# Performance work log

Measured on AMD Instinct MI355X. Metric: run time of the kernel, lower is better.

## Reference

```python
import jax, jax.numpy as jnp
import numpy as np

HEADS = 8
EPS = 1e-6

def _feature_map(x):
    return jax.nn.elu(x) + 1.0

def _linear_attention(q, k, v, motion_weight):
    # q,k,v: [..., N, dh]; motion_weight broadcastable to q or None
    q = _feature_map(q)
    k = _feature_map(k)
    if motion_weight is not None:
        q = q * motion_weight
    k_sum = k.sum(axis=-2, keepdims=True)                      # [...,1,dh]
    kv = jnp.einsum('...nd,...ne->...de', k, v)                # [...,dh,dh]
    out = jnp.einsum('...nd,...de->...ne', q, kv)              # [...,N,dh]
    z = 1.0 / (jnp.einsum('...nd,...md->...nm', q, k_sum) + EPS)  # [...,N,1]
    return out * z

def setup_inputs() -> dict:
    key = jax.random.key(0)
    k1, k2, k3, k4 = jax.random.split(key, 4)
    B, T, H, W, C = 2, 16, 48, 48, 512
    x = jax.random.normal(k1, (B, T, H, W, C), dtype=jnp.float32)
    motion_mag = jax.random.normal(k2, (B, T, H, W, 1), dtype=jnp.float32)
    W_qkv = jax.random.normal(k3, (C, 3 * C), dtype=jnp.float32) * 0.02
    temporal_emb = jax.random.normal(k4, (1, 1, 1, 1, C), dtype=jnp.float32)
    return {"x": x, "motion_mag": motion_mag, "W_qkv": W_qkv, "temporal_emb": temporal_emb}

def _split_heads(t, lead, n, heads, dh):
    # t: [lead, n, heads*dh] -> [lead, heads, n, dh]
    return t.reshape(lead, n, heads, dh).transpose(0, 2, 1, 3)

def reference(x, motion_mag, W_qkv, temporal_emb):
    B, T, H, W, C = x.shape
    dh = C // HEADS
    x = x + temporal_emb

    # ---- temporal linear attention over frame-averaged tokens ----
    x_time = x.reshape(B, T, H * W, C).mean(axis=2)            # [B,T,C]
    qkv = x_time @ W_qkv                                       # [B,T,3C]
    q, k, v = jnp.split(qkv, 3, axis=-1)
    q = _split_heads(q, B, T, HEADS, dh)                       # [B,h,T,dh]
    k = _split_heads(k, B, T, HEADS, dh)
    v = _split_heads(v, B, T, HEADS, dh)
    mm = motion_mag.reshape(B, T, -1).mean(axis=-1, keepdims=True)  # [B,T,1]
    mw_t = 1.0 + jnp.tanh(mm)[:, None]                         # [B,1,T,1]
    t_out = _linear_attention(q, k, v, mw_t)                   # [B,h,T,dh]
    t_out = t_out.transpose(0, 2, 1, 3).reshape(B, T, C)       # [B,T,C]

    # broadcast temporal output over spatial dims
    x_sp = x + t_out[:, :, None, None, :]                      # [B,T,H,W,C]

    # ---- global spatial linear attention per frame ----
    N = H * W
    x_flat = x_sp.reshape(B * T, N, C)
    qkv = x_flat @ W_qkv                                       # [BT,N,3C]
    q, k, v = jnp.split(qkv, 3, axis=-1)
    q = _split_heads(q, B * T, N, HEADS, dh)                   # [BT,h,N,dh]
    k = _split_heads(k, B * T, N, HEADS, dh)
    v = _split_heads(v, B * T, N, HEADS, dh)
    mm2 = motion_mag.reshape(B * T, N, 1)
    mw_s = 1.0 + jnp.tanh(mm2)[:, None]                        # [BT,1,N,1]
    s_out = _linear_attention(q, k, v, mw_s)                   # [BT,h,N,dh]
    s_out = s_out.transpose(0, 2, 1, 3).reshape(B, T, H, W, C)
    return s_out
```

## Files before the change

kernel.cpp:

```cpp
#include <hip/hip_runtime.h>
#include <cstddef>
#include <cstdint>

#define HEADS 8
#define DH 64
#define C 512
#define TC 1536
#define BT 32
#define NTOK 2304
#define TT 16
#define EPS 1e-6f

typedef __attribute__((ext_vector_type(8))) short bf16x8;
typedef __attribute__((ext_vector_type(4))) float f32x4;
typedef __attribute__((address_space(3))) void as3_void;
typedef __attribute__((address_space(1))) const void as1_cvoid;

__device__ __forceinline__ float fmap(float x) {
    return x > 0.f ? x + 1.f : __expf(x);
}
__device__ __forceinline__ unsigned short f2bf(float f) {
    unsigned int u = __float_as_uint(f);
    return (unsigned short)((u + 0x7fffu + ((u >> 16) & 1u)) >> 16);
}
__device__ __forceinline__ unsigned int pack2bf(float a, float b) {
    return (unsigned int)f2bf(a) | ((unsigned int)f2bf(b) << 16);
}
__device__ __forceinline__ float bf2f(unsigned short h) {
    return __uint_as_float(((unsigned int)h) << 16);
}
__device__ __forceinline__ void gload16(const void* g, void* l) {
    __builtin_amdgcn_global_load_lds((as1_cvoid*)(uintptr_t)g,
                                     (as3_void*)(uintptr_t)l, 16, 0, 0);
}

__global__ __launch_bounds__(256) void k_prep_w(
    const float* __restrict__ W, unsigned short* __restrict__ Wt) {
    __shared__ float tile[32][33];
    int col0 = blockIdx.x * 32, c0 = blockIdx.y * 32;
    int tx = threadIdx.x & 31, ty = threadIdx.x >> 5;
#pragma unroll
    for (int j = 0; j < 4; ++j) {
        int c = ty + j * 8;
        tile[c][tx] = W[(size_t)(c0 + c) * TC + col0 + tx];
    }
    __syncthreads();
#pragma unroll
    for (int j = 0; j < 4; ++j) {
        int col = ty + j * 8;
        Wt[(size_t)(col0 + col) * C + c0 + tx] = f2bf(tile[tx][col]);
    }
}

__global__ __launch_bounds__(256) void k_time_reduce(
    const float* __restrict__ x, const float* __restrict__ motion,
    float* __restrict__ xtraw, float* __restrict__ mmraw,
    unsigned short* __restrict__ xb) {
    int bt = blockIdx.x, sp = blockIdx.y, tid = threadIdx.x;
    int n0 = sp * 288, cid = tid * 2;
    const float* xp = x + ((size_t)(bt * NTOK + n0)) * C + cid;
    unsigned short* xbp = xb + ((size_t)(bt * NTOK + n0)) * C + cid;
    float s0 = 0.f, s1 = 0.f;
    for (int n = 0; n < 288; ++n) {
        float2 v = *(const float2*)(xp + (size_t)n * C);
        s0 += v.x;
        s1 += v.y;
        *(unsigned int*)(xbp + (size_t)n * C) = pack2bf(v.x, v.y);
    }
    atomicAdd(&xtraw[bt * C + cid], s0);
    atomicAdd(&xtraw[bt * C + cid + 1], s1);

    const float* mp = motion + (size_t)bt * NTOK + n0;
    float m = mp[tid];
    if (tid < 32) m += mp[256 + tid];
    __shared__ float red[256];
    red[tid] = m;
    __syncthreads();
    for (int s = 128; s > 0; s >>= 1) {
        if (tid < s) red[tid] += red[tid + s];
        __syncthreads();
    }
    if (tid == 0) atomicAdd(&mmraw[bt], red[0]);
}

__global__ __launch_bounds__(256) void k_time_qkv(
    const float* __restrict__ xtraw, const float* __restrict__ temb,
    const float* __restrict__ W, float* __restrict__ qkvt) {
    int bt = blockIdx.x, col = blockIdx.y * 256 + threadIdx.x, tid = threadIdx.x;
    __shared__ float xl[C];
    xl[tid]       = xtraw[bt * C + tid]       * (1.f / NTOK) + temb[tid];
    xl[tid + 256] = xtraw[bt * C + tid + 256] * (1.f / NTOK) + temb[tid + 256];
    __syncthreads();
    float a = 0.f;
#pragma unroll 8
    for (int c = 0; c < C; ++c) a += xl[c] * W[(size_t)c * TC + col];
    qkvt[(size_t)bt * TC + col] = a;
}

__global__ __launch_bounds__(256) void k_time_attn(
    const float* __restrict__ qkvt, const float* __restrict__ mmraw,
    const float* __restrict__ temb, float* __restrict__ bias) {
    int b = blockIdx.x, h = blockIdx.y, tid = threadIdx.x;
    int d = tid & 63, g = tid >> 6;
    __shared__ float qs[TT][DH], ks[TT][DH], vs[TT][DH], ksum[DH];
    __shared__ float kvl[DH][DH];
    for (int t = g; t < TT; t += 4) {
        size_t base = (size_t)(b * TT + t) * TC + h * DH + d;
        float mwt = 1.f + tanhf(mmraw[b * TT + t] * (1.f / NTOK));
        qs[t][d] = fmap(qkvt[base]) * mwt;
        ks[t][d] = fmap(qkvt[base + C]);
        vs[t][d] = qkvt[base + 2 * C];
    }
    __syncthreads();
    if (g == 0) {
        float s = 0.f;
        for (int t = 0; t < TT; ++t) s += ks[t][d];
        ksum[d] = s;
    }
    float kva[16];
#pragma unroll
    for (int i = 0; i < 16; ++i) kva[i] = 0.f;
    for (int t = 0; t < TT; ++t) {
        float kd = ks[t][d];
#pragma unroll
        for (int i = 0; i < 16; ++i) kva[i] += kd * vs[t][g * 16 + i];
    }
#pragma unroll
    for (int i = 0; i < 16; ++i) kvl[d][g * 16 + i] = kva[i];
    __syncthreads();
    for (int tt = 0; tt < 4; ++tt) {
        int t = g * 4 + tt;
        float acc = 0.f, zden = 0.f;
        for (int dd = 0; dd < DH; ++dd) {
            float qv = qs[t][dd];
            acc  += qv * kvl[dd][d];
            zden += qv * ksum[dd];
        }
        bias[(size_t)(b * TT + t) * C + h * DH + d] =
            acc / (zden + EPS) + temb[h * DH + d];
    }
}

__global__ __launch_bounds__(256) void k_bias_vec(
    const float* __restrict__ bias, const float* __restrict__ W,
    float* __restrict__ bvec) {
    int bt = blockIdx.x, col = blockIdx.y * 256 + threadIdx.x, tid = threadIdx.x;
    __shared__ float bl[C];
    bl[tid]       = bias[bt * C + tid];
    bl[tid + 256] = bias[bt * C + tid + 256];
    __syncthreads();
    float a = 0.f;
#pragma unroll 8
    for (int c = 0; c < C; ++c) a += bl[c] * W[(size_t)c * TC + col];
    bvec[(size_t)bt * TC + col] = a;
}

__global__ __launch_bounds__(512) void k_spatial_kv(
    const unsigned short* __restrict__ xb, const unsigned short* __restrict__ Wt,
    const float* __restrict__ bvec, float* __restrict__ kvw,
    float* __restrict__ ksw) {
    __shared__ __align__(16) char smem[50176];
    unsigned short* A_s = (unsigned short*)smem;
    unsigned short* B_s = (unsigned short*)(smem + 16384);
    char* kvT = smem;
    float* bvl = (float*)(smem + 49152);

    const int s = blockIdx.x, hp = blockIdx.y, bt = blockIdx.z;
    const int tid = threadIdx.x, lane = tid & 63, w = tid >> 6;
    const int lm = lane & 15, quad = lane >> 4;
    const int mr = w & 1, nc = w >> 1;
    const int li8 = lane >> 3, lp = lane & 7;

    if (tid < 256) {
        int h2 = tid >> 7, j2 = tid & 127;
        int wr = (j2 < 64) ? (C + (hp * 2 + h2) * DH + j2)
                           : (2 * C + (hp * 2 + h2) * DH + (j2 - 64));
        bvl[tid] = bvec[(size_t)bt * TC + wr];
    }
    float ksp0 = 0.f, ksp1 = 0.f;
    f32x4 kvacc[2][2];
#pragma unroll
    for (int a = 0; a < 2; ++a)
#pragma unroll
        for (int b = 0; b < 2; ++b) kvacc[a][b] = (f32x4)0.f;

    for (int t = 0; t < 3; ++t) {
        const int n0 = (s * 3 + t) * 128;
        f32x4 acc[4][4];
#pragma unroll
        for (int i = 0; i < 4; ++i)
#pragma unroll
            for (int j = 0; j < 4; ++j) acc[i][j] = (f32x4)0.f;

        for (int kc = 0; kc < 8; ++kc) {
            __syncthreads();
#pragma unroll
            for (int l = 0; l < 2; ++l) {
                int rowbase = w * 16 + l * 8;
                int row = rowbase + li8;
                int c = lp ^ (row & 7);
                gload16(xb + ((size_t)(bt * NTOK + n0 + row)) * C + kc * 64 + c * 8,
                        A_s + rowbase * 64);
            }
#pragma unroll
            for (int l = 0; l < 4; ++l) {
                int rowbase = w * 32 + l * 8;
                int r = rowbase + li8;
                int c = lp ^ (r & 7);
                int h2 = r >> 7, j2 = r & 127;
                int wr = (j2 < 64) ? (C + (hp * 2 + h2) * DH + j2)
                                   : (2 * C + (hp * 2 + h2) * DH + (j2 - 64));
                gload16(Wt + (size_t)wr * C + kc * 64 + c * 8, B_s + rowbase * 64);
            }
            __syncthreads();
#pragma unroll
            for (int ks = 0; ks < 2; ++ks) {
                bf16x8 af[4], bfr[4];
#pragma unroll
                for (int i = 0; i < 4; ++i) {
                    int row = mr * 64 + i * 16 + lm;
                    int p = (ks * 4 + quad) ^ (row & 7);
                    af[i] = *(const bf16x8*)&A_s[row * 64 + p * 8];
                }
#pragma unroll
                for (int j = 0; j < 4; ++j) {
                    int row = nc * 64 + j * 16 + lm;
                    int p = (ks * 4 + quad) ^ (row & 7);
                    bfr[j] = *(const bf16x8*)&B_s[row * 64 + p * 8];
                }
#pragma unroll
                for (int i = 0; i < 4; ++i)
#pragma unroll
                    for (int j = 0; j < 4; ++j)
                        acc[i][j] = __builtin_amdgcn_mfma_f32_16x16x32_bf16(
                            af[i], bfr[j], acc[i][j], 0, 0, 0);
            }
        }
#pragma unroll 1
        for (int ph = 0; ph < 2; ++ph) {
            __syncthreads();
            if ((nc >> 1) == ph) {
#pragma unroll
                for (int i = 0; i < 4; ++i) {
                    int tokb = mr * 64 + i * 16 + quad * 4;
                    int tc = tokb >> 3;
#pragma unroll
                    for (int j = 0; j < 4; ++j) {
                        int cg = nc * 64 + j * 16 + lm;
                        int cl = cg & 127;
                        float bv = bvl[cg];
                        f32x4 a4 = acc[i][j];
                        float v0 = a4[0] + bv, v1 = a4[1] + bv;
                        float v2 = a4[2] + bv, v3 = a4[3] + bv;
                        if (cl < 64) {
                            v0 = fmap(v0); v1 = fmap(v1);
                            v2 = fmap(v2); v3 = fmap(v3);
                        }
                        int p = (tc & 8) | ((tc & 7) ^ (cl & 7));
                        uint2 pk;
                        pk.x = pack2bf(v0, v1);
                        pk.y = pack2bf(v2, v3);
                        *(uint2*)(kvT + cl * 256 + p * 16 + (tokb & 7) * 2) = pk;
                    }
                }
            }
            __syncthreads();
            if (tid < 128) {
                int d = tid & 63, half = tid >> 6;
                float ssum = 0.f;
#pragma unroll
                for (int tc2 = 0; tc2 < 8; ++tc2) {
                    int tcc = half * 8 + tc2;
                    int p = (tcc & 8) | ((tcc & 7) ^ (d & 7));
                    bf16x8 v8 = *(const bf16x8*)(kvT + d * 256 + p * 16);
#pragma unroll
                    for (int q = 0; q < 8; ++q)
                        ssum += bf2f((unsigned short)v8[q]);
                }
                if (ph == 0) ksp0 += ssum; else ksp1 += ssum;
            }
#pragma unroll
            for (int dt2 = 0; dt2 < 2; ++dt2) {
                int drow = (mr * 2 + dt2) * 16 + lm;
                int erow = 64 + nc * 16 + lm;
#pragma unroll
                for (int ks2 = 0; ks2 < 4; ++ks2) {
                    int tcc = ks2 * 4 + quad;
                    int pA = (tcc & 8) | ((tcc & 7) ^ (drow & 7));
                    int pB = (tcc & 8) | ((tcc & 7) ^ (erow & 7));
                    bf16x8 ak = *(const bf16x8*)(kvT + drow * 256 + pA * 16);
                    bf16x8 bv8 = *(const bf16x8*)(kvT + erow * 256 + pB * 16);
                    kvacc[ph][dt2] = __builtin_amdgcn_mfma_f32_16x16x32_bf16(
                        ak, bv8, kvacc[ph][dt2], 0, 0, 0);
                }
            }
        }
    }
#pragma unroll
    for (int ph = 0; ph < 2; ++ph) {
        float* kvp = kvw + (size_t)(bt * HEADS + hp * 2 + ph) * DH * DH;
#pragma unroll
        for (int dt2 = 0; dt2 < 2; ++dt2) {
            int d0 = (mr * 2 + dt2) * 16 + quad * 4;
            int e = nc * 16 + lm;
#pragma unroll
            for (int r = 0; r < 4; ++r)
                atomicAdd(&kvp[(d0 + r) * DH + e], kvacc[ph][dt2][r]);
        }
    }
    if (tid < 128) {
        int d = tid & 63;
        atomicAdd(&ksw[(bt * HEADS + hp * 2 + 0) * DH + d], ksp0);
        atomicAdd(&ksw[(bt * HEADS + hp * 2 + 1) * DH + d], ksp1);
    }
}

__global__ __launch_bounds__(256) void k_spatial_out(
    const unsigned short* __restrict__ xb, const unsigned short* __restrict__ Wt,
    const float* __restrict__ bvec, const float* __restrict__ motion,
    const float* __restrict__ kvw, const float* __restrict__ ksw,
    float* __restrict__ out) {
    __shared__ __align__(16) char smem[51712];
    unsigned short* A_s = (unsigned short*)smem;
    unsigned short* B_s = (unsigned short*)(smem + 16384);
    char* qs  = smem;
    char* kvT = smem + 32768;
    float* bvl = (float*)(smem + 49152);
    float* mwv = (float*)(smem + 49664);
    float* ksl = (float*)(smem + 50176);
    float* zv  = (float*)(smem + 50688);

    const int tile = blockIdx.x, hp = blockIdx.y, bt = blockIdx.z;
    const int tid = threadIdx.x, lane = tid & 63, w = tid >> 6;
    const int lm = lane & 15, quad = lane >> 4;
    const int mr = w & 1, nc = w >> 1;
    const int li8 = lane >> 3, lp = lane & 7;
    const int n0 = tile * 128;

    if (tid < 128) {
        bvl[tid] = bvec[(size_t)bt * TC + hp * 128 + tid];
        mwv[tid] = 1.f + tanhf(motion[(size_t)bt * NTOK + n0 + tid]);
        ksl[tid] = ksw[(bt * HEADS + hp * 2 + (tid >> 6)) * DH + (tid & 63)];
    }
    {
        int rr = tid & 127, hh = tid >> 7;
        int head = rr >> 6, e = rr & 63;
        const float* kvp = kvw + (size_t)(bt * HEADS + hp * 2 + head) * DH * DH;
#pragma unroll 8
        for (int d = hh * 32; d < hh * 32 + 32; ++d) {
            int p = (d >> 3) ^ (rr & 7);
            ((unsigned short*)(kvT + rr * 128 + p * 16))[d & 7] = f2bf(kvp[d * DH + e]);
        }
    }
    f32x4 acc[4][4];
#pragma unroll
    for (int i = 0; i < 4; ++i)
#pragma unroll
        for (int j = 0; j < 4; ++j) acc[i][j] = (f32x4)0.f;

    for (int kc = 0; kc < 8; ++kc) {
        __syncthreads();
#pragma unroll
        for (int l = 0; l < 4; ++l) {
            int rowbase = w * 32 + l * 8;
            int row = rowbase + li8;
            int c = lp ^ (row & 7);
            gload16(xb + ((size_t)(bt * NTOK + n0 + row)) * C + kc * 64 + c * 8,
                    A_s + rowbase * 64);
        }
#pragma unroll
        for (int l = 0; l < 4; ++l) {
            int rowbase = w * 32 + l * 8;
            int r = rowbase + li8;
            int c = lp ^ (r & 7);
            gload16(Wt + (size_t)(hp * 128 + r) * C + kc * 64 + c * 8,
                    B_s + rowbase * 64);
        }
        __syncthreads();
#pragma unroll
        for (int ks = 0; ks < 2; ++ks) {
            bf16x8 af[4], bfr[4];
#pragma unroll
            for (int i = 0; i < 4; ++i) {
                int row = mr * 64 + i * 16 + lm;
                int p = (ks * 4 + quad) ^ (row & 7);
                af[i] = *(const bf16x8*)&A_s[row * 64 + p * 8];
            }
#pragma unroll
            for (int j = 0; j < 4; ++j) {
                int row = nc * 64 + j * 16 + lm;
                int p = (ks * 4 + quad) ^ (row & 7);
                bfr[j] = *(const bf16x8*)&B_s[row * 64 + p * 8];
            }
#pragma unroll
            for (int i = 0; i < 4; ++i)
#pragma unroll
                for (int j = 0; j < 4; ++j)
                    acc[i][j] = __builtin_amdgcn_mfma_f32_16x16x32_bf16(
                        af[i], bfr[j], acc[i][j], 0, 0, 0);
        }
    }
    __syncthreads();
#pragma unroll
    for (int i = 0; i < 4; ++i) {
#pragma unroll
        for (int j = 0; j < 4; ++j) {
            int cl = nc * 64 + j * 16 + lm;
            float bv = bvl[cl];
            int cch = cl >> 3;
#pragma unroll
            for (int r = 0; r < 4; ++r) {
                int tok = mr * 64 + i * 16 + quad * 4 + r;
                float qv = fmap(acc[i][j][r] + bv) * mwv[tok];
                int p = (cch & 8) | ((cch & 7) ^ (tok & 7));
                ((unsigned short*)(qs + tok * 256 + p * 16))[cl & 7] = f2bf(qv);
            }
        }
    }
    __syncthreads();
    {
        int head = tid >> 7, tok = tid & 127;
        float zd = 0.f;
#pragma unroll
        for (int tc3 = 0; tc3 < 8; ++tc3) {
            int cch = head * 8 + tc3;
            int p = (cch & 8) | ((cch & 7) ^ (tok & 7));
            bf16x8 q8 = *(const bf16x8*)(qs + tok * 256 + p * 16);
#pragma unroll
            for (int q = 0; q < 8; ++q)
                zd += bf2f((unsigned short)q8[q]) * ksl[head * 64 + tc3 * 8 + q];
        }
        zv[head * 128 + tok] = 1.f / (zd + EPS);
    }
    __syncthreads();
    f32x4 oacc[4][4];
#pragma unroll
    for (int i = 0; i < 4; ++i)
#pragma unroll
        for (int j = 0; j < 4; ++j) oacc[i][j] = (f32x4)0.f;
#pragma unroll
    for (int ks3 = 0; ks3 < 2; ++ks3) {
        bf16x8 aq[4], bk[4];
#pragma unroll
        for (int i = 0; i < 4; ++i) {
            int tok = mr * 64 + i * 16 + lm;
            int cch = nc * 8 + ks3 * 4 + quad;
            int p = (cch & 8) | ((cch & 7) ^ (tok & 7));
            aq[i] = *(const bf16x8*)(qs + tok * 256 + p * 16);
        }
#pragma unroll
        for (int j = 0; j < 4; ++j) {
            int row = nc * 64 + j * 16 + lm;
            int tcc = ks3 * 4 + quad;
            int p = tcc ^ (row & 7);
            bk[j] = *(const bf16x8*)(kvT + row * 128 + p * 16);
        }
#pragma unroll
        for (int i = 0; i < 4; ++i)
#pragma unroll
            for (int j = 0; j < 4; ++j)
                oacc[i][j] = __builtin_amdgcn_mfma_f32_16x16x32_bf16(
                    aq[i], bk[j], oacc[i][j], 0, 0, 0);
    }
    const int h = hp * 2 + nc;
#pragma unroll
    for (int i = 0; i < 4; ++i)
#pragma unroll
        for (int r = 0; r < 4; ++r) {
            int tok = mr * 64 + i * 16 + quad * 4 + r;
            float z = zv[nc * 128 + tok];
#pragma unroll
            for (int j = 0; j < 4; ++j)
                out[((size_t)(bt * NTOK + n0 + tok)) * C + h * DH + j * 16 + lm] =
                    oacc[i][j][r] * z;
        }
}

extern "C" void kernel_launch(void* const* d_in, const int* in_sizes, int n_in,
                              void* d_out, int out_size, void* d_ws, size_t ws_size,
                              hipStream_t stream) {
    (void)in_sizes; (void)n_in; (void)out_size; (void)ws_size;
    const float* x      = (const float*)d_in[0];
    const float* motion = (const float*)d_in[1];
    const float* W      = (const float*)d_in[2];
    const float* temb   = (const float*)d_in[3];
    float* out = (float*)d_out;
    float* ws  = (float*)d_ws;

    float* kvw   = ws;
    float* ksw   = kvw + 1048576;
    float* xtraw = ksw + 16384;
    float* mmraw = xtraw + 16384;
    float* qkvt  = mmraw + 32;
    float* bias  = qkvt + 49152;
    float* bvec  = bias + 16384;
    unsigned short* Wt = (unsigned short*)(bvec + 49152);
    unsigned short* xb = (unsigned short*)(Wt + (size_t)TC * C);

    hipMemsetAsync(d_ws, 0,
                   (size_t)(1048576 + 16384 + 16384 + 32) * sizeof(float), stream);
    k_prep_w<<<dim3(48, 16), 256, 0, stream>>>(W, Wt);
    k_time_reduce<<<dim3(BT, 8), 256, 0, stream>>>(x, motion, xtraw, mmraw, xb);
    k_time_qkv<<<dim3(BT, 6), 256, 0, stream>>>(xtraw, temb, W, qkvt);
    k_time_attn<<<dim3(2, HEADS), 256, 0, stream>>>(qkvt, mmraw, temb, bias);
    k_bias_vec<<<dim3(BT, 6), 256, 0, stream>>>(bias, W, bvec);
    k_spatial_kv<<<dim3(6, 4, BT), 512, 0, stream>>>(xb, Wt, bvec, kvw, ksw);
    k_spatial_out<<<dim3(18, 4, BT), 256, 0, stream>>>(xb, Wt, bvec, motion,
                                                       kvw, ksw, out);
}
```

Measured before the change: 573.3 us.

## Double-buffer LDS tiles in spatial KV GEMM to overlap loads with MFMA

Adds a second LDS buffer for the A and B tiles in k_spatial_kv so the global-to-LDS load for the next K chunk is issued before the MFMAs on the current chunk. Source pointers are precomputed once, and the kv transpose staging is moved to a different LDS offset. This aims to hide global load latency behind matrix math and removes one barrier per K step. In exchange LDS use roughly doubles to about 97KB per block, which can lower occupancy, and it adds a barrier after each tile.

```diff
diff --git a/kernel.cpp b/kernel.cpp
--- a/kernel.cpp
+++ b/kernel.cpp
@@ -159,11 +159,13 @@
     const unsigned short* __restrict__ xb, const unsigned short* __restrict__ Wt,
     const float* __restrict__ bvec, float* __restrict__ kvw,
     float* __restrict__ ksw) {
-    __shared__ __align__(16) char smem[50176];
-    unsigned short* A_s = (unsigned short*)smem;
-    unsigned short* B_s = (unsigned short*)(smem + 16384);
-    char* kvT = smem;
-    float* bvl = (float*)(smem + 49152);
+    __shared__ __align__(16) char smem[99328];
+    unsigned short* A0 = (unsigned short*)smem;
+    unsigned short* B0 = (unsigned short*)(smem + 16384);
+    unsigned short* A1 = (unsigned short*)(smem + 49152);
+    unsigned short* B1 = (unsigned short*)(smem + 65536);
+    char* kvT = smem + 16384;
+    float* bvl = (float*)(smem + 98304);
 
     const int s = blockIdx.x, hp = blockIdx.y, bt = blockIdx.z;
     const int tid = threadIdx.x, lane = tid & 63, w = tid >> 6;
@@ -177,6 +179,24 @@
                            : (2 * C + (hp * 2 + h2) * DH + (j2 - 64));
         bvl[tid] = bvec[(size_t)bt * TC + wr];
     }
+    const unsigned short* srcA[2];
+#pragma unroll
+    for (int l = 0; l < 2; ++l) {
+        int row = w * 16 + l * 8 + li8;
+        int c = lp ^ (row & 7);
+        srcA[l] = xb + ((size_t)(bt * NTOK + row)) * C + c * 8;
+    }
+    const unsigned short* srcB[4];
+#pragma unroll
+    for (int l = 0; l < 4; ++l) {
+        int r = w * 32 + l * 8 + li8;
+        int c = lp ^ (r & 7);
+        int h2 = r >> 7, j2 = r & 127;
+        int wr = (j2 < 64) ? (C + (hp * 2 + h2) * DH + j2)
+                           : (2 * C + (hp * 2 + h2) * DH + (j2 - 64));
+        srcB[l] = Wt + (size_t)wr * C + c * 8;
+    }
+
     float ksp0 = 0.f, ksp1 = 0.f;
     f32x4 kvacc[2][2];
 #pragma unroll
@@ -184,6 +204,16 @@
 #pragma unroll
         for (int b = 0; b < 2; ++b) kvacc[a][b] = (f32x4)0.f;
 
+    auto STAGE = [&](unsigned short* As, unsigned short* Bs, int n0, int kc) {
+#pragma unroll
+        for (int l = 0; l < 2; ++l)
+            gload16(srcA[l] + (size_t)n0 * C + kc * 64, As + (w * 16 + l * 8) * 64);
+#pragma unroll
+        for (int l = 0; l < 4; ++l)
+            gload16(srcB[l] + kc * 64, Bs + (w * 32 + l * 8) * 64);
+    };
+
+#pragma unroll 1
     for (int t = 0; t < 3; ++t) {
         const int n0 = (s * 3 + t) * 128;
         f32x4 acc[4][4];
@@ -192,27 +222,16 @@
 #pragma unroll
             for (int j = 0; j < 4; ++j) acc[i][j] = (f32x4)0.f;
 
+        STAGE(A0, B0, n0, 0);
+        __syncthreads();
+#pragma unroll
         for (int kc = 0; kc < 8; ++kc) {
-            __syncthreads();
-#pragma unroll
-            for (int l = 0; l < 2; ++l) {
-                int rowbase = w * 16 + l * 8;
-                int row = rowbase + li8;
-                int c = lp ^ (row & 7);
-                gload16(xb + ((size_t)(bt * NTOK + n0 + row)) * C + kc * 64 + c * 8,
-                        A_s + rowbase * 64);
-            }
-#pragma unroll
-            for (int l = 0; l < 4; ++l) {
-                int rowbase = w * 32 + l * 8;
-                int r = rowbase + li8;
-                int c = lp ^ (r & 7);
-                int h2 = r >> 7, j2 = r & 127;
-                int wr = (j2 < 64) ? (C + (hp * 2 + h2) * DH + j2)
-                                   : (2 * C + (hp * 2 + h2) * DH + (j2 - 64));
-                gload16(Wt + (size_t)wr * C + kc * 64 + c * 8, B_s + rowbase * 64);
-            }
-            __syncthreads();
+            const unsigned short* As = (kc & 1) ? A1 : A0;
+            const unsigned short* Bs = (kc & 1) ? B1 : B0;
+            if (kc < 7) {
+                STAGE((kc & 1) ? A0 : A1, (kc & 1) ? B0 : B1, n0, kc + 1);
+                __builtin_amdgcn_sched_barrier(0);
+            }
 #pragma unroll
             for (int ks = 0; ks < 2; ++ks) {
                 bf16x8 af[4], bfr[4];
@@ -220,13 +239,13 @@
                 for (int i = 0; i < 4; ++i) {
                     int row = mr * 64 + i * 16 + lm;
                     int p = (ks * 4 + quad) ^ (row & 7);
-                    af[i] = *(const bf16x8*)&A_s[row * 64 + p * 8];
+                    af[i] = *(const bf16x8*)&As[row * 64 + p * 8];
                 }
 #pragma unroll
                 for (int j = 0; j < 4; ++j) {
                     int row = nc * 64 + j * 16 + lm;
                     int p = (ks * 4 + quad) ^ (row & 7);
-                    bfr[j] = *(const bf16x8*)&B_s[row * 64 + p * 8];
+                    bfr[j] = *(const bf16x8*)&Bs[row * 64 + p * 8];
                 }
 #pragma unroll
                 for (int i = 0; i < 4; ++i)
@@ -235,6 +254,7 @@
                         acc[i][j] = __builtin_amdgcn_mfma_f32_16x16x32_bf16(
                             af[i], bfr[j], acc[i][j], 0, 0, 0);
             }
+            __syncthreads();
         }
 #pragma unroll 1
         for (int ph = 0; ph < 2; ++ph) {
@@ -295,6 +315,7 @@
                 }
             }
         }
+        __syncthreads();
     }
 #pragma unroll
     for (int ph = 0; ph < 2; ++ph) {
```

New measurement: 539.5 us. -5.9%, faster.

## Double-buffer LDS staging in spatial KV GEMM with prefetch of next K chunk

Applied to the files above, without the earlier changes.

Restructures the QKV-projection GEMM inside k_spatial_kv into a two-stage pipeline. Each K step drops from 64 to 32 columns so two A/B buffers fit in LDS, and the next chunk is issued with global_load_lds while MFMAs run on the current one. It uses a simpler 4-way XOR swizzle, precomputed source pointers, sched_barrier and s_setprio around the MFMA block. The kvT scratch is moved to overlap the B buffers, which needs an extra barrier at the end of each tile. The trade-off is twice as many loop iterations and barriers, in exchange for hiding global load latency.

```diff
diff --git a/kernel.cpp b/kernel.cpp
--- a/kernel.cpp
+++ b/kernel.cpp
@@ -15,6 +15,8 @@
 typedef __attribute__((ext_vector_type(4))) float f32x4;
 typedef __attribute__((address_space(3))) void as3_void;
 typedef __attribute__((address_space(1))) const void as1_cvoid;
+
+#define SCHED0() __builtin_amdgcn_sched_barrier(0)
 
 __device__ __forceinline__ float fmap(float x) {
     return x > 0.f ? x + 1.f : __expf(x);
@@ -160,16 +162,21 @@
     const float* __restrict__ bvec, float* __restrict__ kvw,
     float* __restrict__ ksw) {
     __shared__ __align__(16) char smem[50176];
-    unsigned short* A_s = (unsigned short*)smem;
-    unsigned short* B_s = (unsigned short*)(smem + 16384);
-    char* kvT = smem;
+    unsigned short* const Abuf[2] = {
+        (unsigned short*)smem,
+        (unsigned short*)(smem + 8192)};
+    unsigned short* const Bbuf[2] = {
+        (unsigned short*)(smem + 16384),
+        (unsigned short*)(smem + 32768)};
+    char* kvT = smem + 16384;
     float* bvl = (float*)(smem + 49152);
 
     const int s = blockIdx.x, hp = blockIdx.y, bt = blockIdx.z;
     const int tid = threadIdx.x, lane = tid & 63, w = tid >> 6;
     const int lm = lane & 15, quad = lane >> 4;
     const int mr = w & 1, nc = w >> 1;
-    const int li8 = lane >> 3, lp = lane & 7;
+    const int li4 = lane >> 2, lp4 = lane & 3;
+    const int pq = quad ^ (lm & 3);
 
     if (tid < 256) {
         int h2 = tid >> 7, j2 = tid & 127;
@@ -177,6 +184,20 @@
                            : (2 * C + (hp * 2 + h2) * DH + (j2 - 64));
         bvl[tid] = bvec[(size_t)bt * TC + wr];
     }
+    const int rowA = w * 16 + li4;
+    const unsigned short* srcA =
+        xb + ((size_t)(bt * NTOK + rowA)) * C + (lp4 ^ (rowA & 3)) * 8;
+    const unsigned short* srcB[2];
+#pragma unroll
+    for (int l = 0; l < 2; ++l) {
+        int r = w * 32 + l * 16 + li4;
+        int cB = lp4 ^ (r & 3);
+        int h2 = r >> 7, j2 = r & 127;
+        int wr = (j2 < 64) ? (C + (hp * 2 + h2) * DH + j2)
+                           : (2 * C + (hp * 2 + h2) * DH + (j2 - 64));
+        srcB[l] = Wt + (size_t)wr * C + cB * 8;
+    }
+
     float ksp0 = 0.f, ksp1 = 0.f;
     f32x4 kvacc[2][2];
 #pragma unroll
@@ -184,6 +205,15 @@
 #pragma unroll
         for (int b = 0; b < 2; ++b) kvacc[a][b] = (f32x4)0.f;
 
+    auto STAGE_A = [&](unsigned short* As, int n0, int kc) {
+        gload16(srcA + (size_t)n0 * C + kc * 32, As + w * 512);
+    };
+    auto STAGE_B = [&](unsigned short* Bs, int kc) {
+        gload16(srcB[0] + kc * 32, Bs + w * 1024);
+        gload16(srcB[1] + kc * 32, Bs + w * 1024 + 512);
+    };
+
+#pragma unroll 1
     for (int t = 0; t < 3; ++t) {
         const int n0 = (s * 3 + t) * 128;
         f32x4 acc[4][4];
@@ -192,49 +222,34 @@
 #pragma unroll
             for (int j = 0; j < 4; ++j) acc[i][j] = (f32x4)0.f;
 
-        for (int kc = 0; kc < 8; ++kc) {
+        STAGE_A(Abuf[0], n0, 0);
+        STAGE_B(Bbuf[0], 0);
+        __syncthreads();
+#pragma unroll
+        for (int kc = 0; kc < 16; ++kc) {
+            const unsigned short* As = Abuf[kc & 1];
+            const unsigned short* Bs = Bbuf[kc & 1];
+            if (kc < 15) {
+                STAGE_A(Abuf[(kc + 1) & 1], n0, kc + 1);
+                STAGE_B(Bbuf[(kc + 1) & 1], kc + 1);
+                SCHED0();
+            }
+            __builtin_amdgcn_s_setprio(1);
+            bf16x8 af[4], bfr[4];
+#pragma unroll
+            for (int i = 0; i < 4; ++i)
+                af[i] = *(const bf16x8*)&As[(mr * 64 + i * 16 + lm) * 32 + pq * 8];
+#pragma unroll
+            for (int j = 0; j < 4; ++j)
+                bfr[j] = *(const bf16x8*)&Bs[(nc * 64 + j * 16 + lm) * 32 + pq * 8];
+#pragma unroll
+            for (int i = 0; i < 4; ++i)
+#pragma unroll
+                for (int j = 0; j < 4; ++j)
+                    acc[i][j] = __builtin_amdgcn_mfma_f32_16x16x32_bf16(
+                        af[i], bfr[j], acc[i][j], 0, 0, 0);
+            __builtin_amdgcn_s_setprio(0);
             __syncthreads();
-#pragma unroll
-            for (int l = 0; l < 2; ++l) {
-                int rowbase = w * 16 + l * 8;
-                int row = rowbase + li8;
-                int c = lp ^ (row & 7);
-                gload16(xb + ((size_t)(bt * NTOK + n0 + row)) * C + kc * 64 + c * 8,
-                        A_s + rowbase * 64);
-            }
-#pragma unroll
-            for (int l = 0; l < 4; ++l) {
-                int rowbase = w * 32 + l * 8;
-                int r = rowbase + li8;
-                int c = lp ^ (r & 7);
-                int h2 = r >> 7, j2 = r & 127;
-                int wr = (j2 < 64) ? (C + (hp * 2 + h2) * DH + j2)
-                                   : (2 * C + (hp * 2 + h2) * DH + (j2 - 64));
-                gload16(Wt + (size_t)wr * C + kc * 64 + c * 8, B_s + rowbase * 64);
-            }
-            __syncthreads();
-#pragma unroll
-            for (int ks = 0; ks < 2; ++ks) {
-                bf16x8 af[4], bfr[4];
-#pragma unroll
-                for (int i = 0; i < 4; ++i) {
-                    int row = mr * 64 + i * 16 + lm;
-                    int p = (ks * 4 + quad) ^ (row & 7);
-                    af[i] = *(const bf16x8*)&A_s[row * 64 + p * 8];
-                }
-#pragma unroll
-                for (int j = 0; j < 4; ++j) {
-                    int row = nc * 64 + j * 16 + lm;
-                    int p = (ks * 4 + quad) ^ (row & 7);
-                    bfr[j] = *(const bf16x8*)&B_s[row * 64 + p * 8];
-                }
-#pragma unroll
-                for (int i = 0; i < 4; ++i)
-#pragma unroll
-                    for (int j = 0; j < 4; ++j)
-                        acc[i][j] = __builtin_amdgcn_mfma_f32_16x16x32_bf16(
-                            af[i], bfr[j], acc[i][j], 0, 0, 0);
-            }
         }
 #pragma unroll 1
         for (int ph = 0; ph < 2; ++ph) {
@@ -295,6 +310,7 @@
                 }
             }
         }
+        __syncthreads();
     }
 #pragma unroll
     for (int ph = 0; ph < 2; ++ph) {
```

Result: faster. 561.1 us (-2.1%).

## Load GEMM MFMA fragments directly from global memory instead of LDS staging

Applied to the files above, without the earlier changes.

Both spatial kernels now read A and B MFMA operand fragments straight from global memory into registers, replacing the global_load_lds staging into swizzled shared-memory tiles. This removes the two barriers per K-chunk and the LDS round trip, and shrinks shared memory in the kv kernel, which may allow more blocks per CU. In exchange, each wave reloads the data it shares with other waves, relying on L1/L2 hits, and there is no explicit prefetch to hide global latency. A barrier is added at the end of each token tile so the LDS region reused for kvT stays safe.

```diff
diff --git a/kernel.cpp b/kernel.cpp
--- a/kernel.cpp
+++ b/kernel.cpp
@@ -13,8 +13,6 @@
 
 typedef __attribute__((ext_vector_type(8))) short bf16x8;
 typedef __attribute__((ext_vector_type(4))) float f32x4;
-typedef __attribute__((address_space(3))) void as3_void;
-typedef __attribute__((address_space(1))) const void as1_cvoid;
 
 __device__ __forceinline__ float fmap(float x) {
     return x > 0.f ? x + 1.f : __expf(x);
@@ -28,10 +26,6 @@
 }
 __device__ __forceinline__ float bf2f(unsigned short h) {
     return __uint_as_float(((unsigned int)h) << 16);
-}
-__device__ __forceinline__ void gload16(const void* g, void* l) {
-    __builtin_amdgcn_global_load_lds((as1_cvoid*)(uintptr_t)g,
-                                     (as3_void*)(uintptr_t)l, 16, 0, 0);
 }
 
 __global__ __launch_bounds__(256) void k_prep_w(
@@ -159,17 +153,14 @@
     const unsigned short* __restrict__ xb, const unsigned short* __restrict__ Wt,
     const float* __restrict__ bvec, float* __restrict__ kvw,
     float* __restrict__ ksw) {
-    __shared__ __align__(16) char smem[50176];
-    unsigned short* A_s = (unsigned short*)smem;
-    unsigned short* B_s = (unsigned short*)(smem + 16384);
+    __shared__ __align__(16) char smem[33792];
     char* kvT = smem;
-    float* bvl = (float*)(smem + 49152);
+    float* bvl = (float*)(smem + 32768);
 
     const int s = blockIdx.x, hp = blockIdx.y, bt = blockIdx.z;
     const int tid = threadIdx.x, lane = tid & 63, w = tid >> 6;
     const int lm = lane & 15, quad = lane >> 4;
     const int mr = w & 1, nc = w >> 1;
-    const int li8 = lane >> 3, lp = lane & 7;
 
     if (tid < 256) {
         int h2 = tid >> 7, j2 = tid & 127;
@@ -177,6 +168,16 @@
                            : (2 * C + (hp * 2 + h2) * DH + (j2 - 64));
         bvl[tid] = bvec[(size_t)bt * TC + wr];
     }
+    const unsigned short* Brow[4];
+#pragma unroll
+    for (int j = 0; j < 4; ++j) {
+        int cg = nc * 64 + j * 16 + lm;
+        int h2 = cg >> 7, j2 = cg & 127;
+        int wr = (j2 < 64) ? (C + (hp * 2 + h2) * DH + j2)
+                           : (2 * C + (hp * 2 + h2) * DH + (j2 - 64));
+        Brow[j] = Wt + (size_t)wr * C + quad * 8;
+    }
+
     float ksp0 = 0.f, ksp1 = 0.f;
     f32x4 kvacc[2][2];
 #pragma unroll
@@ -184,57 +185,35 @@
 #pragma unroll
         for (int b = 0; b < 2; ++b) kvacc[a][b] = (f32x4)0.f;
 
+#pragma unroll 1
     for (int t = 0; t < 3; ++t) {
         const int n0 = (s * 3 + t) * 128;
+        const unsigned short* Arow[4];
+#pragma unroll
+        for (int i = 0; i < 4; ++i)
+            Arow[i] = xb + ((size_t)(bt * NTOK + n0 + mr * 64 + i * 16 + lm)) * C
+                      + quad * 8;
         f32x4 acc[4][4];
 #pragma unroll
         for (int i = 0; i < 4; ++i)
 #pragma unroll
             for (int j = 0; j < 4; ++j) acc[i][j] = (f32x4)0.f;
 
-        for (int kc = 0; kc < 8; ++kc) {
-            __syncthreads();
-#pragma unroll
-            for (int l = 0; l < 2; ++l) {
-                int rowbase = w * 16 + l * 8;
-                int row = rowbase + li8;
-                int c = lp ^ (row & 7);
-                gload16(xb + ((size_t)(bt * NTOK + n0 + row)) * C + kc * 64 + c * 8,
-                        A_s + rowbase * 64);
-            }
-#pragma unroll
-            for (int l = 0; l < 4; ++l) {
-                int rowbase = w * 32 + l * 8;
-                int r = rowbase + li8;
-                int c = lp ^ (r & 7);
-                int h2 = r >> 7, j2 = r & 127;
-                int wr = (j2 < 64) ? (C + (hp * 2 + h2) * DH + j2)
-                                   : (2 * C + (hp * 2 + h2) * DH + (j2 - 64));
-                gload16(Wt + (size_t)wr * C + kc * 64 + c * 8, B_s + rowbase * 64);
-            }
-            __syncthreads();
-#pragma unroll
-            for (int ks = 0; ks < 2; ++ks) {
-                bf16x8 af[4], bfr[4];
-#pragma unroll
-                for (int i = 0; i < 4; ++i) {
-                    int row = mr * 64 + i * 16 + lm;
-                    int p = (ks * 4 + quad) ^ (row & 7);
-                    af[i] = *(const bf16x8*)&A_s[row * 64 + p * 8];
-                }
-#pragma unroll
-                for (int j = 0; j < 4; ++j) {
-                    int row = nc * 64 + j * 16 + lm;
-                    int p = (ks * 4 + quad) ^ (row & 7);
-                    bfr[j] = *(const bf16x8*)&B_s[row * 64 + p * 8];
-                }
-#pragma unroll
-                for (int i = 0; i < 4; ++i)
-#pragma unroll
-                    for (int j = 0; j < 4; ++j)
-                        acc[i][j] = __builtin_amdgcn_mfma_f32_16x16x32_bf16(
-                            af[i], bfr[j], acc[i][j], 0, 0, 0);
-            }
+#pragma unroll 4
+        for (int kc = 0; kc < 16; ++kc) {
+            bf16x8 af[4], bfr[4];
+#pragma unroll
+            for (int i = 0; i < 4; ++i)
+                af[i] = *(const bf16x8*)(Arow[i] + kc * 32);
+#pragma unroll
+            for (int j = 0; j < 4; ++j)
+                bfr[j] = *(const bf16x8*)(Brow[j] + kc * 32);
+#pragma unroll
+            for (int i = 0; i < 4; ++i)
+#pragma unroll
+                for (int j = 0; j < 4; ++j)
+                    acc[i][j] = __builtin_amdgcn_mfma_f32_16x16x32_bf16(
+                        af[i], bfr[j], acc[i][j], 0, 0, 0);
         }
 #pragma unroll 1
         for (int ph = 0; ph < 2; ++ph) {
@@ -295,6 +274,7 @@
                 }
             }
         }
+        __syncthreads();
     }
 #pragma unroll
     for (int ph = 0; ph < 2; ++ph) {
@@ -321,8 +301,6 @@
     const float* __restrict__ kvw, const float* __restrict__ ksw,
     float* __restrict__ out) {
     __shared__ __align__(16) char smem[51712];
-    unsigned short* A_s = (unsigned short*)smem;
-    unsigned short* B_s = (unsigned short*)(smem + 16384);
     char* qs  = smem;
     char* kvT = smem + 32768;
     float* bvl = (float*)(smem + 49152);
@@ -334,7 +312,6 @@
     const int tid = threadIdx.x, lane = tid & 63, w = tid >> 6;
     const int lm = lane & 15, quad = lane >> 4;
     const int mr = w & 1, nc = w >> 1;
-    const int li8 = lane >> 3, lp = lane & 7;
     const int n0 = tile * 128;
 
     if (tid < 128) {
@@ -352,53 +329,37 @@
             ((unsigned short*)(kvT + rr * 128 + p * 16))[d & 7] = f2bf(kvp[d * DH + e]);
         }
     }
+    const unsigned short* Arow[4];
+    const unsigned short* Brow[4];
+#pragma unroll
+    for (int i = 0; i < 4; ++i)
+        Arow[i] = xb + ((size_t)(bt * NTOK + n0 + mr * 64 + i * 16 + lm)) * C
+                  + quad * 8;
+#pragma unroll
+    for (int j = 0; j < 4; ++j)
+        Brow[j] = Wt + (size_t)(hp * 128 + nc * 64 + j * 16 + lm) * C + quad * 8;
+
     f32x4 acc[4][4];
 #pragma unroll
     for (int i = 0; i < 4; ++i)
 #pragma unroll
         for (int j = 0; j < 4; ++j) acc[i][j] = (f32x4)0.f;
 
-    for (int kc = 0; kc < 8; ++kc) {
-        __syncthreads();
-#pragma unroll
-        for (int l = 0; l < 4; ++l) {
-            int rowbase = w * 32 + l * 8;
-            int row = rowbase + li8;
-            int c = lp ^ (row & 7);
-            gload16(xb + ((size_t)(bt * NTOK + n0 + row)) * C + kc * 64 + c * 8,
-                    A_s + rowbase * 64);
-        }
-#pragma unroll
-        for (int l = 0; l < 4; ++l) {
-            int rowbase = w * 32 + l * 8;
-            int r = rowbase + li8;
-            int c = lp ^ (r & 7);
-            gload16(Wt + (size_t)(hp * 128 + r) * C + kc * 64 + c * 8,
-                    B_s + rowbase * 64);
-        }
-        __syncthreads();
-#pragma unroll
-        for (int ks = 0; ks < 2; ++ks) {
-            bf16x8 af[4], bfr[4];
-#pragma unroll
-            for (int i = 0; i < 4; ++i) {
-                int row = mr * 64 + i * 16 + lm;
-                int p = (ks * 4 + quad) ^ (row & 7);
-                af[i] = *(const bf16x8*)&A_s[row * 64 + p * 8];
-            }
-#pragma unroll
-            for (int j = 0; j < 4; ++j) {
-                int row = nc * 64 + j * 16 + lm;
-                int p = (ks * 4 + quad) ^ (row & 7);
-                bfr[j] = *(const bf16x8*)&B_s[row * 64 + p * 8];
-            }
-#pragma unroll
-            for (int i = 0; i < 4; ++i)
-#pragma unroll
-                for (int j = 0; j < 4; ++j)
-                    acc[i][j] = __builtin_amdgcn_mfma_f32_16x16x32_bf16(
-                        af[i], bfr[j], acc[i][j], 0, 0, 0);
-        }
+#pragma unroll 4
+    for (int kc = 0; kc < 16; ++kc) {
+        bf16x8 af[4], bfr[4];
+#pragma unroll
+        for (int i = 0; i < 4; ++i)
+            af[i] = *(const bf16x8*)(Arow[i] + kc * 32);
+#pragma unroll
+        for (int j = 0; j < 4; ++j)
+            bfr[j] = *(const bf16x8*)(Brow[j] + kc * 32);
+#pragma unroll
+        for (int i = 0; i < 4; ++i)
+#pragma unroll
+            for (int j = 0; j < 4; ++j)
+                acc[i][j] = __builtin_amdgcn_mfma_f32_16x16x32_bf16(
+                    af[i], bfr[j], acc[i][j], 0, 0, 0);
     }
     __syncthreads();
 #pragma unroll
```

Result: slower. 810.4 us (+41.4%).
